# Performance work log

Measured on AMD Instinct MI355X. Metric: run time of the kernel, lower is better.

Reference implementation:

```python
import jax, jax.numpy as jnp
import numpy as np

V, D, H, H2 = 50000, 256, 128, 128
B, S, T1 = 8, 512, 101
GAMMA = 1.0

def setup_inputs():
    key = jax.random.key(0)
    ks = jax.random.split(key, 24)
    g = lambda i, shape: jax.random.normal(ks[i], shape, jnp.float32) * 0.05
    z = lambda n: jnp.zeros((n,), jnp.float32)
    return dict(
        text=jax.random.randint(ks[0], (B, S), 0, V),
        text_length=jax.random.randint(ks[1], (B,), S // 2, S + 1),
        summary=jax.random.randint(ks[2], (B, T1), 0, V),
        summary_length=jax.random.randint(ks[3], (B,), 20, T1 + 1),
        word_vectors=g(4, (V, D)),
        Wih_f=g(5, (4 * H, D)), Whh_f=g(6, (4 * H, H)), bih_f=z(4 * H), bhh_f=z(4 * H),
        Wih_b=g(7, (4 * H, D)), Whh_b=g(8, (4 * H, H)), bih_b=z(4 * H), bhh_b=z(4 * H),
        Wdih=g(9, (4 * H, D)), Wdhh=g(10, (4 * H, H)), bdih=z(4 * H), bdhh=z(4 * H),
        W1=g(11, (H2, 3 * H + 1)), b1=z(H2),
        W2=g(12, (1, H2)), b2=z(1),
        Wl=g(13, (V, 3 * H)), bl=z(V),
    )

def _lstm_cell(x, h, c, Wih, Whh, bih, bhh):
    # torch gate order: i, f, g, o
    gates = x @ Wih.T + h @ Whh.T + bih + bhh
    i, f, g, o = jnp.split(gates, 4, axis=-1)
    c_new = jax.nn.sigmoid(f) * c + jax.nn.sigmoid(i) * jnp.tanh(g)
    h_new = jax.nn.sigmoid(o) * jnp.tanh(c_new)
    return h_new, c_new

def _masked_lstm(x, mask, Wih, Whh, bih, bhh):
    # emulate packed sequence: state frozen and output zeroed past each length
    Bsz, Hh = x.shape[0], Whh.shape[1]
    def step(carry, inp):
        h, c = carry
        xt, mt = inp
        h_new, c_new = _lstm_cell(xt, h, c, Wih, Whh, bih, bhh)
        m = mt[:, None]
        return (jnp.where(m, h_new, h), jnp.where(m, c_new, c)), jnp.where(m, h_new, 0.0)
    init = (jnp.zeros((Bsz, Hh), x.dtype), jnp.zeros((Bsz, Hh), x.dtype))
    (h, c), out = jax.lax.scan(step, init, (x.transpose(1, 0, 2), mask.T))
    return out.transpose(1, 0, 2), h, c  # out: [B,S,H]

def _forward(text, text_length, summary, summary_length, word_vectors, Wih_f, Whh_f, bih_f, bhh_f, Wih_b, Whh_b, bih_b, bhh_b, Wdih, Wdhh, bdih, bdhh, W1, b1, W2, b2, Wl, bl):
    Bsz, Slen = text.shape
    pos = jnp.arange(Slen)
    mask = pos[None, :] < text_length[:, None]  # [B,S]
    emb = word_vectors[text]  # [B,S,D]
    # bidirectional encoder (layer 0 fwd state initializes decoder, as h[:,0])
    out_f, h0, c0 = _masked_lstm(emb, mask, Wih_f, Whh_f, bih_f, bhh_f)
    ridx = jnp.where(mask, text_length[:, None] - 1 - pos[None, :], pos[None, :])
    x_rev = jnp.take_along_axis(emb, ridx[:, :, None], axis=1)
    out_r, _, _ = _masked_lstm(x_rev, mask, Wih_b, Whh_b, bih_b, bhh_b)
    out_b = jnp.take_along_axis(out_r, ridx[:, :, None], axis=1) * mask[:, :, None]
    text_states = jnp.concatenate([out_f, out_b], -1)  # [B,S,2H]

    T = summary.shape[1] - 1
    def dec_step(carry, inp):
        h, c, cov, loss = carry
        tok_t, tok_tp1, valid = inp
        x = word_vectors[tok_t]
        h_new, c_new = _lstm_cell(x, h, c, Wdih, Wdhh, bdih, bdhh)
        hs = jnp.broadcast_to(h_new[:, None, :], (text_states.shape[0], text_states.shape[1], h_new.shape[-1]))
        feats = jnp.concatenate([text_states, hs, cov[:, :, None]], -1)  # [B,S,3H+1]
        hid = jnp.tanh(jnp.einsum('bsf,hf->bsh', feats, W1) + b1)
        scores = jnp.einsum('bsh,oh->bso', hid, W2)[..., 0] + b2[0]  # [B,S]
        attn = jax.nn.softmax(scores, axis=-1)
        context = jnp.einsum('bs,bsd->bd', attn, text_states)  # [B,2H]
        logits = jnp.concatenate([context, h_new], -1) @ Wl.T + bl
        logp = jax.nn.log_softmax(logits, -1)
        nll = -jnp.take_along_axis(logp, tok_tp1[:, None], axis=1)[:, 0]
        cov_loss = jnp.minimum(cov, attn).sum(-1)  # min over cat([cov, attn], -2), summed
        step_loss = jnp.where(valid, nll + GAMMA * cov_loss, 0.0).sum()
        vm = valid[:, None]
        h = jnp.where(vm, h_new, h)
        c = jnp.where(vm, c_new, c)
        cov = cov + jnp.where(vm, attn, 0.0)  # coverage accumulated every step in supervised path
        return (h, c, cov, loss + step_loss), None
    tok_t = summary[:, :-1].T  # [T,B]
    tok_tp1 = summary[:, 1:].T
    valid = summary_length[None, :] > (jnp.arange(T)[:, None] + 1)  # summary_length - t - 1 > 0
    carry0 = (h0, c0, jnp.zeros((text_states.shape[0], text_states.shape[1]), jnp.float32), jnp.zeros((), jnp.float32))
    (h, c, cov, loss), _ = jax.lax.scan(dec_step, carry0, (tok_t, tok_tp1, valid))
    return loss / T

def reference(text, text_length, summary, summary_length, word_vectors, Wih_f, Whh_f, bih_f, bhh_f, Wih_b, Whh_b, bih_b, bhh_b, Wdih, Wdhh, bdih, bdhh, W1, b1, W2, b2, Wl, bl):
    return _forward(text, text_length, summary, summary_length, word_vectors, Wih_f, Whh_f, bih_f, bhh_f, Wih_b, Whh_b, bih_b, bhh_b, Wdih, Wdhh, bdih, bdhh, W1, b1, W2, b2, Wl, bl)
```

## Files before the change

### kernel.cpp

```cpp
#include <hip/hip_runtime.h>
#include <hip/hip_bf16.h>

#define VV 50000
#define DD 256
#define HH 128
#define G4 512
#define BB 8
#define SS 512
#define TT 100
#define T1 101
#define GAMMA 1.0f
#define LOG2E 1.44269504f
#define CGB 224
#define TPB 14
#define NBLK (17+CGB)

#define KB 10
#define NAB (TT/KB)
#define NIT (NAB+3)
#define AT_M 31
#define CX_M 31
#define HN_M 31
#define CV_M 63
#define PM_M 31

__device__ inline float rcpf_(float x){
#if __has_builtin(__builtin_amdgcn_rcpf)
  return __builtin_amdgcn_rcpf(x);
#else
  return 1.0f/x;
#endif
}
__device__ inline float exp2f_(float x){
#if __has_builtin(__builtin_amdgcn_exp2f)
  return __builtin_amdgcn_exp2f(x);
#else
  return exp2f(x);
#endif
}
__device__ inline float log2f_(float x){
#if __has_builtin(__builtin_amdgcn_logf)
  return __builtin_amdgcn_logf(x);
#else
  return log2f(x);
#endif
}
__device__ inline float fexp(float x){ return exp2f_(x*LOG2E); }
__device__ inline float sigf(float x){ return rcpf_(1.f + exp2f_(-x*LOG2E)); }
__device__ inline float tanh_(float x){
  float e = exp2f_(x*(2.0f*LOG2E));
  return 1.0f - 2.0f*rcpf_(e+1.0f);
}
__device__ inline unsigned short f2bf(float x){
  unsigned u = __float_as_uint(x);
  return (unsigned short)((u + 0x7fffu + ((u>>16)&1u)) >> 16);
}
__device__ inline float bf2f(unsigned short s){ return __uint_as_float(((unsigned)s)<<16); }
__device__ inline float bfrnd(float x){
  return __uint_as_float((__float_as_uint(x)+0x8000u)&0xffff0000u);
}
__device__ inline unsigned pack2rq(float a, float b){
#if __has_builtin(__builtin_amdgcn_perm)
  unsigned ua = __float_as_uint(a) + 0x8000u;
  unsigned ub = __float_as_uint(b) + 0x8000u;
  return __builtin_amdgcn_perm(ub, ua, 0x07060302u);
#else
  unsigned ra = (__float_as_uint(a)+0x8000u)>>16;
  unsigned rb = (__float_as_uint(b)+0x8000u)>>16;
  return ra | (rb<<16);
#endif
}

typedef __attribute__((ext_vector_type(2))) _Float16 h2v;
typedef __attribute__((ext_vector_type(8))) short bfrag;
typedef __attribute__((ext_vector_type(4))) float cfrag;

__device__ inline unsigned packh2(float a, float b){
  unsigned short ha = __builtin_bit_cast(unsigned short, (_Float16)a);
  unsigned short hb = __builtin_bit_cast(unsigned short, (_Float16)b);
  return (unsigned)ha | ((unsigned)hb<<16);
}
__device__ inline float fdot2_(unsigned a, unsigned b, float c){
#if __has_builtin(__builtin_amdgcn_fdot2)
  return __builtin_amdgcn_fdot2(__builtin_bit_cast(h2v, a), __builtin_bit_cast(h2v, b), c, false);
#else
  h2v av = __builtin_bit_cast(h2v, a), bv = __builtin_bit_cast(h2v, b);
  return c + (float)av.x*(float)bv.x + (float)av.y*(float)bv.y;
#endif
}
__device__ inline float hlo(unsigned u){ return (float)__builtin_bit_cast(h2v, u).x; }
__device__ inline float hhi(unsigned u){ return (float)__builtin_bit_cast(h2v, u).y; }

__device__ inline void gbar(unsigned* bar){
  __syncthreads();
  if (threadIdx.x == 0){
    __threadfence();
    int g = blockIdx.x & 7;
    unsigned gsz = (unsigned)((NBLK + 7 - g) >> 3);
    unsigned gen = __hip_atomic_load(bar+576, __ATOMIC_RELAXED, __HIP_MEMORY_SCOPE_AGENT);
    unsigned old = __hip_atomic_fetch_add(bar+64*g, 1u, __ATOMIC_ACQ_REL, __HIP_MEMORY_SCOPE_AGENT);
    if (old == gsz-1u){
      __hip_atomic_store(bar+64*g, 0u, __ATOMIC_RELAXED, __HIP_MEMORY_SCOPE_AGENT);
      unsigned go = __hip_atomic_fetch_add(bar+512, 1u, __ATOMIC_ACQ_REL, __HIP_MEMORY_SCOPE_AGENT);
      if (go == 7u){
        __hip_atomic_store(bar+512, 0u, __ATOMIC_RELAXED, __HIP_MEMORY_SCOPE_AGENT);
        __hip_atomic_fetch_add(bar+576, 1u, __ATOMIC_RELEASE, __HIP_MEMORY_SCOPE_AGENT);
      } else {
        while (__hip_atomic_load(bar+576, __ATOMIC_RELAXED, __HIP_MEMORY_SCOPE_AGENT) == gen)
          __builtin_amdgcn_s_sleep(2);
      }
    } else {
      while (__hip_atomic_load(bar+576, __ATOMIC_RELAXED, __HIP_MEMORY_SCOPE_AGENT) == gen)
        __builtin_amdgcn_s_sleep(2);
    }
    __threadfence();
  }
  __syncthreads();
}

__global__ void __launch_bounds__(256) k_prep_small(
    const float* Wih_f, const float* Wih_b, const float* Whh_f, const float* Whh_b,
    const float* W1, const float* Wdhh,
    float* WihT_f, float* WihT_b, unsigned* W2T_f, unsigned* W2T_b,
    float* W1aT, float* W1c, unsigned* W1h2, unsigned* Wdh2T){
  int i = blockIdx.x*256 + threadIdx.x;
  if (i < 131072){ int k = i>>9, j = i&511; WihT_f[i] = Wih_f[j*DD + k]; return; }
  i -= 131072;
  if (i < 131072){ int k = i>>9, j = i&511; WihT_b[i] = Wih_b[j*DD + k]; return; }
  i -= 131072;
  if (i < 32768){ int k2 = i>>9, j = i&511;
    W2T_f[i] = packh2(Whh_f[j*HH + 2*k2], Whh_f[j*HH + 2*k2+1]); return; }
  i -= 32768;
  if (i < 32768){ int k2 = i>>9, j = i&511;
    W2T_b[i] = packh2(Whh_b[j*HH + 2*k2], Whh_b[j*HH + 2*k2+1]); return; }
  i -= 32768;
  if (i < 32768){ int d = i>>7, k = i&127; W1aT[i] = W1[k*385 + d]; return; }
  i -= 32768;
  if (i < 128){ W1c[i] = W1[i*385 + 384]; return; }
  i -= 128;
  if (i < 8192){ int j2 = i>>7, col = i&127;
    W1h2[i] = packh2(W1[col*385 + 256 + 2*j2], W1[col*385 + 256 + 2*j2+1]); return; }
  i -= 8192;
  if (i < 32768){ int q = i>>9, jj = i&511;
    Wdh2T[i] = packh2(Wdhh[jj*HH + 2*q], Wdhh[jj*HH + 2*q+1]); return; }
}

__global__ void __launch_bounds__(512) k_xd(const int* summary, const float* wv,
    const float* Wdih, const float* bdih, const float* bdhh,
    float* Xd, unsigned* bar){
  __shared__ float xsl[8][256];
  int t = blockIdx.x, tid = threadIdx.x;
  for (int f=tid; f<2048; f+=512){
    int b = f>>8, k = f&255;
    xsl[b][k] = wv[(size_t)summary[b*T1 + t]*DD + k];
  }
  if (blockIdx.x==0){ for (int f=tid; f<1024; f+=512) bar[f] = 0u; }
  __syncthreads();
  int jj = tid;
  float base = bdih[jj] + bdhh[jj];
  const float4* wr = (const float4*)(Wdih + (size_t)jj*DD);
  float acc[8];
  #pragma unroll
  for (int b=0;b<8;b++) acc[b]=0.f;
  for (int q=0;q<64;q++){
    float4 w = wr[q];
    #pragma unroll
    for (int b=0;b<8;b++)
      acc[b] += w.x*xsl[b][4*q] + w.y*xsl[b][4*q+1] + w.z*xsl[b][4*q+2] + w.w*xsl[b][4*q+3];
  }
  #pragma unroll
  for (int b=0;b<8;b++) Xd[((size_t)t*BB + b)*G4 + jj] = base + acc[b];
}

__global__ void k_embed(const int* text, const int* tlen, const float* wv,
                        float* emb, int* ridx){
  int blk = blockIdx.x;
  int b = blk>>9, s = blk&511;
  int tok = text[blk];
  const float4* src = (const float4*)(wv + (size_t)tok*DD);
  float4* dst = (float4*)(emb + (size_t)blk*DD);
  dst[threadIdx.x] = src[threadIdx.x];
  if (threadIdx.x==0){ int len = tlen[b]; ridx[blk] = (s < len) ? (len-1-s) : s; }
}

__global__ void __launch_bounds__(256) k_xgemm(const float* emb, const int* ridx,
    const float* WihT, const float* bi, const float* bh, float* X, int rev){
  __shared__ float e_l[8][256];
  int tid = threadIdx.x;
  int g0 = blockIdx.x*8;
  int b = g0>>9;
  for (int r=0;r<8;r++){
    int s = (g0+r)&511;
    int src = rev ? ridx[b*SS + s] : s;
    e_l[r][tid] = emb[((size_t)(b*SS+src))*DD + tid];
  }
  __syncthreads();
  int j0 = tid, j1 = tid+256;
  float acc0[8], acc1[8];
  #pragma unroll
  for (int r=0;r<8;r++){ acc0[r]=0.f; acc1[r]=0.f; }
  for (int k=0;k<256;k++){
    float w0 = WihT[k*G4 + j0];
    float w1 = WihT[k*G4 + j1];
    #pragma unroll
    for (int r=0;r<8;r++){ float e = e_l[r][k]; acc0[r] += e*w0; acc1[r] += e*w1; }
  }
  float bb0 = bi[j0]+bh[j0], bb1 = bi[j1]+bh[j1];
  for (int r=0;r<8;r++){
    X[((size_t)(g0+r))*G4 + j0] = acc0[r] + bb0;
    X[((size_t)(g0+r))*G4 + j1] = acc1[r] + bb1;
  }
}

__global__ void __launch_bounds__(512) k_encoder(const float* Xf, const float* Xb,
    const unsigned* W2Tf, const unsigned* W2Tb, const int* tlen,
    float* out_f, float* out_r, float* h0, float* c0){
  __shared__ float g_l[512];
  __shared__ __align__(16) unsigned h2_l[64];
  int tid = threadIdx.x;
  int b = blockIdx.x, dir = blockIdx.y;
  const float* X = dir ? Xb : Xf;
  const unsigned* WT = dir ? W2Tb : W2Tf;
  float* out = dir ? out_r : out_f;
  unsigned w[64];
  #pragma unroll
  for (int k2=0;k2<64;k2++) w[k2] = WT[k2*G4 + tid];
  if (tid < 64) h2_l[tid] = 0u;
  float creg = 0.f, hreg = 0.f;
  int len = tlen[b];
  __syncthreads();
  for (int t0=0;t0<len;t0+=8){
    float x8[8];
    #pragma unroll
    for (int i=0;i<8;i++) x8[i] = X[(size_t)(b*SS+t0+i)*G4 + tid];
    float out8[8];
    #pragma unroll
    for (int i=0;i<8;i++){
      int t = t0+i;
      if (t >= len) break;
      float a0 = x8[i], a1 = 0.f, a2 = 0.f, a3 = 0.f;
      const uint4* h4 = (const uint4*)h2_l;
      #pragma unroll
      for (int q=0;q<16;q++){
        uint4 hv = h4[q];
        a0 = fdot2_(w[4*q+0], hv.x, a0);
        a1 = fdot2_(w[4*q+1], hv.y, a1);
        a2 = fdot2_(w[4*q+2], hv.z, a2);
        a3 = fdot2_(w[4*q+3], hv.w, a3);
      }
      g_l[tid] = (a0+a1)+(a2+a3);
      __syncthreads();
      if (tid < 128){
        float ii = sigf(g_l[tid]);
        float ff = sigf(g_l[128+tid]);
        float gg = tanh_(g_l[256+tid]);
        float oo = sigf(g_l[384+tid]);
        creg = ff*creg + ii*gg;
        float hn = oo*tanh_(creg);
        out8[i] = hn;
        hreg = hn;
        ((_Float16*)h2_l)[tid] = (_Float16)hn;
      }
      __syncthreads();
    }
    if (tid < 128){
      int nend = (len - t0 < 8) ? (len - t0) : 8;
      #pragma unroll 8
      for (int i=0;i<nend;i++) out[((size_t)(b*SS+t0+i))*HH + tid] = out8[i];
    }
  }
  if (dir==0 && tid<128){ h0[b*HH+tid]=hreg; c0[b*HH+tid]=creg; }
  for (int f = tid; f < (SS-len)*HH; f += 512){
    int s = len + (f>>7), j = f&127;
    out[((size_t)(b*SS+s))*HH + j] = 0.f;
  }
}

__global__ void __launch_bounds__(256) k_post(const float* out_f, const float* out_r,
    const int* ridx, const float* W1aT, unsigned* ts_h, unsigned* TS1Th){
  __shared__ float ts_l[128*33 + 64];
  int tid = threadIdx.x;
  int b = blockIdx.x, chunk = blockIdx.y;
  int s0 = chunk*32;
  for (int it=0; it<32; ++it){
    int s = s0 + it;
    int d = tid;
    float v;
    if (d < 128) v = out_f[((size_t)(b*SS+s))*HH + d];
    else        v = out_r[((size_t)(b*SS + ridx[b*SS+s]))*HH + (d-128)];
    ts_l[it*256 + d] = v;
  }
  __syncthreads();
  for (int f=tid; f<16*256; f+=256){
    int it2 = f>>8, d = f&255;
    unsigned p = packh2(ts_l[(2*it2)*256 + d], ts_l[(2*it2+1)*256 + d]);
    ts_h[((((size_t)b*2 + (s0>>8))*128) + (((s0&255)>>1) + it2))*256 + d] = p;
  }
  int k = tid & 127, half = tid >> 7;
  float acc[16];
  #pragma unroll
  for (int i=0;i<16;i++) acc[i]=0.f;
  for (int d=0;d<256;d++){
    float w = W1aT[d*128 + k];
    #pragma unroll
    for (int i=0;i<16;i++) acc[i] += ts_l[(half*16+i)*256 + d]*w;
  }
  __syncthreads();
  #pragma unroll
  for (int i=0;i<16;i++) ts_l[k*33 + half*16 + i] = acc[i];
  __syncthreads();
  for (int f=tid; f<64*32; f+=256){
    int k2 = f>>5, sl = f&31;
    unsigned p = packh2(ts_l[(2*k2)*33 + sl], ts_l[(2*k2+1)*33 + sl]);
    TS1Th[((size_t)b*64 + k2)*512 + (s0 + sl)] = p;
  }
}

struct PArgs {
  const int* summary; const int* slen;
  const float* Xd; const unsigned* TS1Th; const unsigned* ts_h;
  const unsigned* W1h2g; const float* W1c; const float* W2; const float* b1;
  const unsigned* Wdh2T; const float* Wl; const float* bl;
  const float* h0; const float* c0;
  float* hn; float* ctx; float* attn; float* covloss;
  float* pm; float* ps; unsigned* bar; float* out;
};

struct __align__(16) LdsAB {
  unsigned W1h2[8192];
  float gates[512];
  float hnl[128], hml[128];
  unsigned hn2[64], hm2[64];
  float4 uhwc[64];
  float2 w2p[64];
  float wredB[8], wredC[8];
};
struct LdsCG { unsigned short xs[16*392]; float rm[64], rs[64]; };
struct LdsCTX { float at[512]; float part[512]; };
struct LdsCB { float tgt[32*BB]; float red[8]; float loss; };
union LdsU { LdsAB ab; LdsCG cg; LdsCTX cx; LdsCB cb; };

__global__ void __launch_bounds__(512,2) k_decode(PArgs a){
  __shared__ LdsU L;
  int bid = blockIdx.x, tid = threadIdx.x;

  if (bid < 8){
    int b = bid;
    int slenb = a.slen[b];
    float b1r = (tid < 128) ? a.b1[tid] : 0.f;
    if (tid < 64){
      L.ab.uhwc[tid] = make_float4(0.f, 0.f, a.W1c[2*tid], a.W1c[2*tid+1]);
      L.ab.w2p[tid]  = make_float2(a.W2[2*tid], a.W2[2*tid+1]);
    }
    for (int f=tid; f<8192; f+=512) L.ab.W1h2[f] = a.W1h2g[f];
    unsigned ts2[64];
    #pragma unroll
    for (int k2=0;k2<64;k2++) ts2[k2] = a.TS1Th[((size_t)b*64 + k2)*512 + tid];
    unsigned wdh[64];
    #pragma unroll
    for (int q=0;q<64;q++) wdh[q] = a.Wdh2T[q*512 + tid];
    float creg = 0.f, hmreg = 0.f;
    if (tid < 128){
      creg  = a.c0[b*HH+tid];
      hmreg = a.h0[b*HH+tid];
      L.ab.hml[tid] = hmreg;
    }
    float cv = 0.f;
    __syncthreads();
    if (tid < 64) L.ab.hm2[tid] = packh2(L.ab.hml[2*tid], L.ab.hml[2*tid+1]);
    __syncthreads();
    {
      const uint4* h4 = (const uint4*)L.ab.hm2;
      float g0 = a.Xd[(size_t)0*BB*G4 + b*G4 + tid], g1 = 0.f, g2 = 0.f, g3 = 0.f;
      #pragma unroll
      for (int q=0;q<16;q++){
        uint4 hv = h4[q];
        g0 = fdot2_(wdh[4*q+0], hv.x, g0);
        g1 = fdot2_(wdh[4*q+1], hv.y, g1);
        g2 = fdot2_(wdh[4*q+2], hv.z, g2);
        g3 = fdot2_(wdh[4*q+3], hv.w, g3);
      }
      L.ab.gates[tid] = (g0+g1)+(g2+g3);
    }
    __syncthreads();

    for (int it=0; it<NIT; ++it){
      if (it < NAB){
        #pragma unroll 1
        for (int j=0;j<KB;j++){
          int t = KB*it + j;
          if (j) __syncthreads();
          if (t >= TT) break;
          int tn = (t+1 < TT) ? t+1 : 0;
          float xdn = a.Xd[(size_t)tn*BB*G4 + b*G4 + tid];
          bool valid = (slenb > t+1);
          if (tid < 128){
            float gi = L.ab.gates[tid];
            float gf = L.ab.gates[128+tid];
            float gg = L.ab.gates[256+tid];
            float go = L.ab.gates[384+tid];
            float ii = sigf(gi), ff = sigf(gf), g2 = tanh_(gg), oo = sigf(go);
            float cn = ff*creg + ii*g2;
            float hv = oo*tanh_(cn);
            if (valid) creg = cn;
            hmreg = valid ? hv : hmreg;
            L.ab.hnl[tid] = hv;
            L.ab.hml[tid] = hmreg;
            a.hn[((size_t)(t&HN_M)*BB + b)*HH + tid] = hv;
          }
          __syncthreads();
          if (tid < 64){
            L.ab.hn2[tid] = packh2(L.ab.hnl[2*tid], L.ab.hnl[2*tid+1]);
            L.ab.hm2[tid] = packh2(L.ab.hml[2*tid], L.ab.hml[2*tid+1]);
          }
          __syncthreads();
          if (tid < 128){
            const uint4* n4 = (const uint4*)L.ab.hn2;
            float u0 = b1r, u1 = 0.f, u2 = 0.f, u3 = 0.f;
            #pragma unroll
            for (int q=0;q<16;q++){
              uint4 nv = n4[q];
              u0 = fdot2_(L.ab.W1h2[(4*q+0)*128+tid], nv.x, u0);
              u1 = fdot2_(L.ab.W1h2[(4*q+1)*128+tid], nv.y, u1);
              u2 = fdot2_(L.ab.W1h2[(4*q+2)*128+tid], nv.z, u2);
              u3 = fdot2_(L.ab.W1h2[(4*q+3)*128+tid], nv.w, u3);
            }
            ((float*)L.ab.uhwc)[(tid>>1)*4 + (tid&1)] = (u0+u1)+(u2+u3);
          }
          __syncthreads();
          float sc0 = 0.f, sc1 = 0.f;
          #pragma unroll
          for (int k2=0;k2<64;k2++){
            unsigned tp = ts2[k2];
            float4 uw  = L.ab.uhwc[k2];
            float2 w2v = L.ab.w2p[k2];
            float p0 = hlo(tp) + uw.x + cv*uw.z;
            float p1 = hhi(tp) + uw.y + cv*uw.w;
            sc0 += tanh_(p0)*w2v.x;
            sc1 += tanh_(p1)*w2v.y;
          }
          float e = fexp(sc0 + sc1);
          int wid = tid>>6;
          float es = e;
          #pragma unroll
          for (int off=32;off>=1;off>>=1) es += __shfl_xor(es, off, 64);
          if ((tid&63)==0) L.ab.wredB[wid] = es;
          __syncthreads();
          float ssum = 0.f;
          #pragma unroll
          for (int w8=0;w8<8;w8++) ssum += L.ab.wredB[w8];
          float at = e * rcpf_(ssum);
          a.attn[((size_t)(t&AT_M)*BB + b)*SS + tid] = at;
          float cl = fminf(cv, at);
          #pragma unroll
          for (int off=32;off>=1;off>>=1) cl += __shfl_xor(cl, off, 64);
          if ((tid&63)==0) L.ab.wredC[wid] = cl;
          __syncthreads();
          if (tid==0){
            float cvs = 0.f;
            #pragma unroll
            for (int w8=0;w8<8;w8++) cvs += L.ab.wredC[w8];
            a.covloss[(t&CV_M)*BB + b] = cvs;
          }
          if (valid) cv += at;
          if (t+1 < TT){
            const uint4* h4 = (const uint4*)L.ab.hm2;
            float g0 = xdn, g1 = 0.f, g2 = 0.f, g3 = 0.f;
            #pragma unroll
            for (int q=0;q<16;q++){
              uint4 hv = h4[q];
              g0 = fdot2_(wdh[4*q+0], hv.x, g0);
              g1 = fdot2_(wdh[4*q+1], hv.y, g1);
              g2 = fdot2_(wdh[4*q+2], hv.z, g2);
              g3 = fdot2_(wdh[4*q+3], hv.w, g3);
            }
            __syncthreads();
            L.ab.gates[tid] = (g0+g1)+(g2+g3);
          }
        }
      }
      gbar(a.bar);
    }
  } else if (bid < 16){
    int b = bid-8;
    int d = tid & 255, half = tid >> 8;
    unsigned tsr[128];
    #pragma unroll
    for (int s2=0;s2<128;s2++)
      tsr[s2] = a.ts_h[((((size_t)b*2 + half)*128) + s2)*256 + d];
    for (int it=0; it<NIT; ++it){
      if (it >= 1 && it <= NAB){
        #pragma unroll 1
        for (int j=0;j<KB;j++){
          int s = KB*(it-1) + j;
          if (s >= TT) break;
          L.cx.at[tid] = a.attn[((size_t)(s&AT_M)*BB + b)*SS + tid];
          __syncthreads();
          float acc = 0.f;
          const float* ap = L.cx.at + half*256;
          #pragma unroll
          for (int s2=0;s2<128;s2++){
            float2 av = *(const float2*)&ap[2*s2];
            unsigned tp = tsr[s2];
            acc += hlo(tp)*av.x + hhi(tp)*av.y;
          }
          L.cx.part[tid] = acc;
          __syncthreads();
          if (tid < 256)
            a.ctx[((size_t)(s&CX_M)*BB + b)*256 + tid] = L.cx.part[tid] + L.cx.part[256+tid];
        }
      }
      gbar(a.bar);
    }
  } else if (bid == 16){
    int b = tid >> 6, l = tid & 63;
    int slenb = a.slen[b];
    if (tid == 0) L.cb.loss = 0.f;
    __syncthreads();
    for (int it=0; it<NIT; ++it){
      #pragma unroll 1
      for (int j=0;j<KB;j++){
        int ts = KB*(it-2) + j;
        if (ts >= 0 && ts < TT){
          int tp = a.summary[b*T1 + ts+1];
          float acc = 0.f;
          #pragma unroll
          for (int i=0;i<6;i++){
            int k = l + 64*i;
            float x = (k < 256) ? a.ctx[((size_t)(ts&CX_M)*BB + b)*256 + k]
                                : a.hn[((size_t)(ts&HN_M)*BB + b)*HH + (k-256)];
            float w = a.Wl[(size_t)tp*384 + k];
            acc += bf2f(f2bf(x)) * bfrnd(w);
          }
          #pragma unroll
          for (int off=32;off>=1;off>>=1) acc += __shfl_xor(acc, off, 64);
          if (l==0) L.cb.tgt[(ts&31)*BB + b] = acc + a.bl[tp];
        }
        int cs = KB*(it-3) + j;
        if (cs >= 0 && cs < TT){
          int slot = cs&PM_M;
          const float* pmp = a.pm + (size_t)slot*BB*CGB + b*CGB;
          const float* psp = a.ps + (size_t)slot*BB*CGB + b*CGB;
          float m = -1e30f;
          for (int jb=l; jb<CGB; jb+=64) m = fmaxf(m, pmp[jb]);
          #pragma unroll
          for (int off=32;off>=1;off>>=1) m = fmaxf(m, __shfl_xor(m, off, 64));
          float s = 0.f;
          for (int jb=l; jb<CGB; jb+=64) s += psp[jb]*fexp(pmp[jb]-m);
          #pragma unroll
          for (int off=32;off>=1;off>>=1) s += __shfl_xor(s, off, 64);
          __syncthreads();
          if (l==0){
            float lse = m + log2f_(s)*0.6931472f;
            bool val = slenb > cs+1;
            L.cb.red[b] = val ? (lse - L.cb.tgt[(cs&31)*BB+b] + GAMMA*a.covloss[(cs&CV_M)*BB+b]) : 0.f;
          }
          __syncthreads();
          if (tid==0){
            float sum = 0.f;
            #pragma unroll
            for (int b2=0;b2<BB;b2++) sum += L.cb.red[b2];
            L.cb.loss += sum;
          }
        }
      }
      if (it==NIT-1 && tid==0) a.out[0] = L.cb.loss*(1.0f/TT);
      gbar(a.bar);
    }
  } else {
    int cb = bid-17;
    int lane = tid & 63, wid = tid >> 6;
    int quad = lane >> 4, col = lane & 15;
    uint4 wreg[24];
    float biasv[2];
    bool nOK[2];
    #pragma unroll
    for (int lt=0; lt<2; lt++){
      int lti = lt*8 + wid;
      bool gv = (lti < TPB);
      int g = cb*TPB + (gv ? lti : 0);
      int n = g*16 + col;
      int nc = (n < VV) ? n : (VV-1);
      const float* wr0 = a.Wl + (size_t)nc*384 + quad*8;
      #pragma unroll
      for (int ks=0; ks<12; ks++){
        float4 w0 = *((const float4*)(wr0 + ks*32));
        float4 w1 = *((const float4*)(wr0 + ks*32 + 4));
        wreg[lt*12+ks] = make_uint4(pack2rq(w0.x,w0.y), pack2rq(w0.z,w0.w),
                                    pack2rq(w1.x,w1.y), pack2rq(w1.z,w1.w));
      }
      nOK[lt] = gv && (n < VV);
      biasv[lt] = nOK[lt] ? a.bl[n] : 0.f;
    }
    for (int it=0; it<NIT; ++it){
      if (it >= 2 && it <= NAB+1){
        #pragma unroll 1
        for (int j=0;j<KB;j++){
          int s = KB*(it-2) + j;
          if (s >= TT) break;
          for (int f=tid; f<16*384; f+=512){
            int m2 = f/384, k = f - m2*384;
            float v = 0.f;
            if (m2 < 8) v = (k < 256) ? a.ctx[((size_t)(s&CX_M)*BB + m2)*256 + k]
                                      : a.hn[((size_t)(s&HN_M)*BB + m2)*HH + (k-256)];
            L.cg.xs[m2*392 + k] = f2bf(v);
          }
          __syncthreads();
          const unsigned short* ap = L.cg.xs + col*392 + quad*8;
          float mr[4], sr[4];
          #pragma unroll
          for (int r=0;r<4;r++){ mr[r] = -1e30f; sr[r] = 0.f; }
          #pragma unroll
          for (int lt=0; lt<2; lt++){
            cfrag acc; acc.x=0.f; acc.y=0.f; acc.z=0.f; acc.w=0.f;
            #pragma unroll
            for (int ks=0; ks<12; ks++){
              bfrag af = *((const bfrag*)(ap + ks*32));
              bfrag bf = __builtin_bit_cast(bfrag, wreg[lt*12+ks]);
              acc = __builtin_amdgcn_mfma_f32_16x16x32_bf16(af, bf, acc, 0,0,0);
            }
            #pragma unroll
            for (int r=0;r<4;r++){
              int mrow = quad*4 + r;
              float v = (mrow < 8 && nOK[lt]) ? (acc[r]+biasv[lt]) : -1e30f;
              float nm = fmaxf(mr[r], v);
              float ev = (v <= -1e29f) ? 0.f : fexp(v-nm);
              sr[r] = sr[r]*fexp(mr[r]-nm) + ev;
              mr[r] = nm;
            }
          }
          #pragma unroll
          for (int off=1; off<16; off<<=1){
            #pragma unroll
            for (int r=0;r<4;r++){
              float m2 = __shfl_xor(mr[r], off, 64);
              float s2 = __shfl_xor(sr[r], off, 64);
              float nm = fmaxf(mr[r], m2);
              sr[r] = sr[r]*fexp(mr[r]-nm) + s2*fexp(m2-nm);
              mr[r] = nm;
            }
          }
          if (col==0 && quad<2){
            #pragma unroll
            for (int r=0;r<4;r++){
              L.cg.rm[wid*8 + quad*4 + r] = mr[r];
              L.cg.rs[wid*8 + quad*4 + r] = sr[r];
            }
          }
          __syncthreads();
          if (tid < 8){
            float M = -1e30f, S = 0.f;
            #pragma unroll
            for (int w8=0; w8<8; w8++){
              float m2 = L.cg.rm[w8*8+tid], s2 = L.cg.rs[w8*8+tid];
              float nm = fmaxf(M, m2);
              S = S*fexp(M-nm) + s2*fexp(m2-nm);
              M = nm;
            }
            a.pm[(size_t)(s&PM_M)*BB*CGB + tid*CGB + cb] = M;
            a.ps[(size_t)(s&PM_M)*BB*CGB + tid*CGB + cb] = S;
          }
        }
      }
      gbar(a.bar);
    }
  }
}

extern "C" void kernel_launch(void* const* d_in, const int* in_sizes, int n_in,
                              void* d_out, int out_size, void* d_ws, size_t ws_size,
                              hipStream_t stream){
  const int* text      = (const int*)d_in[0];
  const int* tlen      = (const int*)d_in[1];
  const int* summary   = (const int*)d_in[2];
  const int* slen      = (const int*)d_in[3];
  const float* wv      = (const float*)d_in[4];
  const float* Wih_f   = (const float*)d_in[5];
  const float* Whh_f   = (const float*)d_in[6];
  const float* bih_f   = (const float*)d_in[7];
  const float* bhh_f   = (const float*)d_in[8];
  const float* Wih_b   = (const float*)d_in[9];
  const float* Whh_b   = (const float*)d_in[10];
  const float* bih_b   = (const float*)d_in[11];
  const float* bhh_b   = (const float*)d_in[12];
  const float* Wdih    = (const float*)d_in[13];
  const float* Wdhh    = (const float*)d_in[14];
  const float* bdih    = (const float*)d_in[15];
  const float* bdhh    = (const float*)d_in[16];
  const float* W1      = (const float*)d_in[17];
  const float* b1      = (const float*)d_in[18];
  const float* W2      = (const float*)d_in[19];
  const float* Wl      = (const float*)d_in[21];
  const float* bl      = (const float*)d_in[22];

  char* ws = (char*)d_ws;
  size_t off = 0;
  auto alloc = [&](size_t n)->void*{
    off = (off + 255) & ~(size_t)255;
    void* p = ws + off; off += n; return p;
  };

  unsigned* W1h2   = (unsigned*)alloc((size_t)8192*4);
  unsigned* Wdh2T  = (unsigned*)alloc((size_t)64*512*4);
  float*    Xd     = (float*)alloc((size_t)TT*BB*G4*4);
  unsigned* ts_h   = (unsigned*)alloc((size_t)BB*2*128*256*4);
  unsigned* TS1Th  = (unsigned*)alloc((size_t)BB*64*512*4);
  float* W1c       = (float*)alloc((size_t)128*4);
  float* h0        = (float*)alloc(BB*HH*4);
  float* c0        = (float*)alloc(BB*HH*4);
  float* hn        = (float*)alloc((size_t)(HN_M+1)*BB*HH*4);
  float* ctx       = (float*)alloc((size_t)(CX_M+1)*BB*256*4);
  float* attn      = (float*)alloc((size_t)(AT_M+1)*BB*SS*4);
  float* covloss   = (float*)alloc((size_t)(CV_M+1)*BB*4);
  float* pm        = (float*)alloc((size_t)(PM_M+1)*BB*CGB*4);
  float* ps        = (float*)alloc((size_t)(PM_M+1)*BB*CGB*4);
  unsigned* bar    = (unsigned*)alloc(4096);

  float* emb     = (float*)alloc((size_t)BB*SS*DD*4);
  float* Xf      = (float*)alloc(((size_t)BB*SS*G4 + 8*G4)*4);
  float* Xb      = (float*)alloc(((size_t)BB*SS*G4 + 8*G4)*4);
  float* WihT_f  = (float*)alloc((size_t)256*512*4);
  float* WihT_b  = (float*)alloc((size_t)256*512*4);
  unsigned* W2T_f= (unsigned*)alloc((size_t)64*512*4);
  unsigned* W2T_b= (unsigned*)alloc((size_t)64*512*4);
  float* out_f   = (float*)alloc((size_t)BB*SS*HH*4);
  float* out_r   = (float*)alloc((size_t)BB*SS*HH*4);
  float* W1aT    = (float*)alloc((size_t)256*128*4);
  int*   ridx    = (int*)  alloc((size_t)BB*SS*4);

  k_prep_small<<<1569,256,0,stream>>>(Wih_f,Wih_b,Whh_f,Whh_b,W1,Wdhh,
                                      WihT_f,WihT_b,W2T_f,W2T_b,W1aT,W1c,W1h2,Wdh2T);
  k_xd<<<TT,512,0,stream>>>(summary, wv, Wdih, bdih, bdhh, Xd, bar);
  k_embed<<<BB*SS,64,0,stream>>>(text, tlen, wv, emb, ridx);
  k_xgemm<<<512,256,0,stream>>>(emb, ridx, WihT_f, bih_f, bhh_f, Xf, 0);
  k_xgemm<<<512,256,0,stream>>>(emb, ridx, WihT_b, bih_b, bhh_b, Xb, 1);
  k_encoder<<<dim3(8,2),512,0,stream>>>(Xf,Xb,W2T_f,W2T_b,tlen,out_f,out_r,h0,c0);
  k_post<<<dim3(8,16),256,0,stream>>>(out_f,out_r,ridx,W1aT,ts_h,TS1Th);

  PArgs a;
  a.summary=summary; a.slen=slen;
  a.Xd=Xd; a.TS1Th=TS1Th; a.ts_h=ts_h;
  a.W1h2g=W1h2; a.W1c=W1c; a.W2=W2; a.b1=b1;
  a.Wdh2T=Wdh2T; a.Wl=Wl; a.bl=bl;
  a.h0=h0; a.c0=c0;
  a.hn=hn; a.ctx=ctx; a.attn=attn; a.covloss=covloss;
  a.pm=pm; a.ps=ps; a.bar=bar; a.out=(float*)d_out;

  k_decode<<<NBLK,512,0,stream>>>(a);
}
```

Baseline: 1.492 ms.

## Split decoder attention score across paired blocks with flag-based handoff

Adds 8 helper blocks, one per batch row, that compute the attention scores for hidden units 72..127 while the main recurrent block computes units 0..71. The two blocks exchange partial scores and the packed hidden state through global memory, synchronised by per-batch release/acquire tags. The serial per-step attention tanh loop on the critical path gets shorter. The macro-step size KB also grows from 10 to 25 and the ring buffers are enlarged to match, so grid barriers happen less often. In exchange, every step now pays two cross-block polling handoffs.

```diff
diff --git a/kernel.cpp b/kernel.cpp
--- a/kernel.cpp
+++ b/kernel.cpp
@@ -13,16 +13,22 @@
 #define LOG2E 1.44269504f
 #define CGB 224
 #define TPB 14
-#define NBLK (17+CGB)
-
-#define KB 10
+#define NBLK (17+8+CGB)
+
+#define KB 25
 #define NAB (TT/KB)
 #define NIT (NAB+3)
-#define AT_M 31
-#define CX_M 31
-#define HN_M 31
-#define CV_M 63
-#define PM_M 31
+#define AT_M 63
+#define CX_M 63
+#define HN_M 127
+#define CV_M 127
+#define PM_M 63
+
+#define A_K2 36
+#define B_K2 (64-A_K2)
+#define THN 640
+#define TGA 768
+#define TGB 896
 
 __device__ inline float rcpf_(float x){
 #if __has_builtin(__builtin_amdgcn_rcpf)
@@ -90,6 +96,16 @@
 }
 __device__ inline float hlo(unsigned u){ return (float)__builtin_bit_cast(h2v, u).x; }
 __device__ inline float hhi(unsigned u){ return (float)__builtin_bit_cast(h2v, u).y; }
+
+__device__ inline void tag_pub(unsigned* tag, unsigned v){
+  __threadfence();
+  __hip_atomic_store(tag, v, __ATOMIC_RELEASE, __HIP_MEMORY_SCOPE_AGENT);
+}
+__device__ inline void tag_poll(unsigned* tag, unsigned v){
+  while (__hip_atomic_load(tag, __ATOMIC_RELAXED, __HIP_MEMORY_SCOPE_AGENT) < v)
+    __builtin_amdgcn_s_sleep(1);
+  __threadfence();
+}
 
 __device__ inline void gbar(unsigned* bar){
   __syncthreads();
@@ -324,6 +340,7 @@
   const float* h0; const float* c0;
   float* hn; float* ctx; float* attn; float* covloss;
   float* pm; float* ps; unsigned* bar; float* out;
+  unsigned* hnG; float* scA; float* scB;
 };
 
 struct __align__(16) LdsAB {
@@ -337,7 +354,7 @@
 };
 struct LdsCG { unsigned short xs[16*392]; float rm[64], rs[64]; };
 struct LdsCTX { float at[512]; float part[512]; };
-struct LdsCB { float tgt[32*BB]; float red[8]; float loss; };
+struct LdsCB { float tgt[64*BB]; float red[8]; float loss; };
 union LdsU { LdsAB ab; LdsCG cg; LdsCTX cx; LdsCB cb; };
 
 __global__ void __launch_bounds__(512,2) k_decode(PArgs a){
@@ -347,15 +364,15 @@
   if (bid < 8){
     int b = bid;
     int slenb = a.slen[b];
-    float b1r = (tid < 128) ? a.b1[tid] : 0.f;
+    float b1r = (tid < 2*A_K2) ? a.b1[tid] : 0.f;
     if (tid < 64){
       L.ab.uhwc[tid] = make_float4(0.f, 0.f, a.W1c[2*tid], a.W1c[2*tid+1]);
       L.ab.w2p[tid]  = make_float2(a.W2[2*tid], a.W2[2*tid+1]);
     }
     for (int f=tid; f<8192; f+=512) L.ab.W1h2[f] = a.W1h2g[f];
-    unsigned ts2[64];
-    #pragma unroll
-    for (int k2=0;k2<64;k2++) ts2[k2] = a.TS1Th[((size_t)b*64 + k2)*512 + tid];
+    unsigned ts2[A_K2];
+    #pragma unroll
+    for (int k2=0;k2<A_K2;k2++) ts2[k2] = a.TS1Th[((size_t)b*64 + k2)*512 + tid];
     unsigned wdh[64];
     #pragma unroll
     for (int q=0;q<64;q++) wdh[q] = a.Wdh2T[q*512 + tid];
@@ -410,11 +427,14 @@
           }
           __syncthreads();
           if (tid < 64){
-            L.ab.hn2[tid] = packh2(L.ab.hnl[2*tid], L.ab.hnl[2*tid+1]);
+            unsigned pn = packh2(L.ab.hnl[2*tid], L.ab.hnl[2*tid+1]);
+            L.ab.hn2[tid] = pn;
+            a.hnG[((size_t)b*2 + (t&1))*64 + tid] = pn;
             L.ab.hm2[tid] = packh2(L.ab.hml[2*tid], L.ab.hml[2*tid+1]);
           }
           __syncthreads();
-          if (tid < 128){
+          if (tid == 504) tag_pub(a.bar + THN + 16*b, (unsigned)(t+1));
+          if (tid < 2*A_K2){
             const uint4* n4 = (const uint4*)L.ab.hn2;
             float u0 = b1r, u1 = 0.f, u2 = 0.f, u3 = 0.f;
             #pragma unroll
@@ -430,7 +450,7 @@
           __syncthreads();
           float sc0 = 0.f, sc1 = 0.f;
           #pragma unroll
-          for (int k2=0;k2<64;k2++){
+          for (int k2=0;k2<A_K2;k2++){
             unsigned tp = ts2[k2];
             float4 uw  = L.ab.uhwc[k2];
             float2 w2v = L.ab.w2p[k2];
@@ -439,7 +459,14 @@
             sc0 += tanh_(p0)*w2v.x;
             sc1 += tanh_(p1)*w2v.y;
           }
-          float e = fexp(sc0 + sc1);
+          float scA = sc0 + sc1;
+          a.scA[((size_t)b*2 + (t&1))*512 + tid] = scA;
+          __syncthreads();
+          if (tid == 504) tag_pub(a.bar + TGA + 16*b, (unsigned)(t+1));
+          if (tid == 0)   tag_poll(a.bar + TGB + 16*b, (unsigned)(t+1));
+          __syncthreads();
+          float sc = scA + a.scB[((size_t)b*2 + (t&1))*512 + tid];
+          float e = fexp(sc);
           int wid = tid>>6;
           float es = e;
           #pragma unroll
@@ -534,7 +561,7 @@
           }
           #pragma unroll
           for (int off=32;off>=1;off>>=1) acc += __shfl_xor(acc, off, 64);
-          if (l==0) L.cb.tgt[(ts&31)*BB + b] = acc + a.bl[tp];
+          if (l==0) L.cb.tgt[(ts&63)*BB + b] = acc + a.bl[tp];
         }
         int cs = KB*(it-3) + j;
         if (cs >= 0 && cs < TT){
@@ -553,7 +580,7 @@
           if (l==0){
             float lse = m + log2f_(s)*0.6931472f;
             bool val = slenb > cs+1;
-            L.cb.red[b] = val ? (lse - L.cb.tgt[(cs&31)*BB+b] + GAMMA*a.covloss[(cs&CV_M)*BB+b]) : 0.f;
+            L.cb.red[b] = val ? (lse - L.cb.tgt[(cs&63)*BB+b] + GAMMA*a.covloss[(cs&CV_M)*BB+b]) : 0.f;
           }
           __syncthreads();
           if (tid==0){
@@ -567,8 +594,84 @@
       if (it==NIT-1 && tid==0) a.out[0] = L.cb.loss*(1.0f/TT);
       gbar(a.bar);
     }
+  } else if (bid < 25){
+    int b = bid-17;
+    int slenb = a.slen[b];
+    float b1r2 = (tid < 2*B_K2) ? a.b1[2*A_K2 + tid] : 0.f;
+    if (tid < 64){
+      L.ab.uhwc[tid] = make_float4(0.f, 0.f, a.W1c[2*tid], a.W1c[2*tid+1]);
+      L.ab.w2p[tid]  = make_float2(a.W2[2*tid], a.W2[2*tid+1]);
+    }
+    for (int f=tid; f<8192; f+=512) L.ab.W1h2[f] = a.W1h2g[f];
+    unsigned ts2b[B_K2];
+    #pragma unroll
+    for (int i=0;i<B_K2;i++) ts2b[i] = a.TS1Th[((size_t)b*64 + (A_K2+i))*512 + tid];
+    float cv = 0.f;
+    __syncthreads();
+    for (int it=0; it<NIT; ++it){
+      if (it < NAB){
+        #pragma unroll 1
+        for (int j=0;j<KB;j++){
+          int t = KB*it + j;
+          if (t >= TT) break;
+          if (tid == 0) tag_poll(a.bar + THN + 16*b, (unsigned)(t+1));
+          __syncthreads();
+          if (tid < 64) L.ab.hn2[tid] = a.hnG[((size_t)b*2 + (t&1))*64 + tid];
+          __syncthreads();
+          if (tid < 2*B_K2){
+            int col = 2*A_K2 + tid;
+            const uint4* n4 = (const uint4*)L.ab.hn2;
+            float u0 = b1r2, u1 = 0.f, u2 = 0.f, u3 = 0.f;
+            #pragma unroll
+            for (int q=0;q<16;q++){
+              uint4 nv = n4[q];
+              u0 = fdot2_(L.ab.W1h2[(4*q+0)*128+col], nv.x, u0);
+              u1 = fdot2_(L.ab.W1h2[(4*q+1)*128+col], nv.y, u1);
+              u2 = fdot2_(L.ab.W1h2[(4*q+2)*128+col], nv.z, u2);
+              u3 = fdot2_(L.ab.W1h2[(4*q+3)*128+col], nv.w, u3);
+            }
+            ((float*)L.ab.uhwc)[(col>>1)*4 + (col&1)] = (u0+u1)+(u2+u3);
+          }
+          __syncthreads();
+          float sc0 = 0.f, sc1 = 0.f;
+          #pragma unroll
+          for (int i=0;i<B_K2;i++){
+            int k2 = A_K2 + i;
+            unsigned tp = ts2b[i];
+            float4 uw  = L.ab.uhwc[k2];
+            float2 w2v = L.ab.w2p[k2];
+            float p0 = hlo(tp) + uw.x + cv*uw.z;
+            float p1 = hhi(tp) + uw.y + cv*uw.w;
+            sc0 += tanh_(p0)*w2v.x;
+            sc1 += tanh_(p1)*w2v.y;
+          }
+          float scB = sc0 + sc1;
+          a.scB[((size_t)b*2 + (t&1))*512 + tid] = scB;
+          __syncthreads();
+          if (tid == 504) tag_pub(a.bar + TGB + 16*b, (unsigned)(t+1));
+          if (tid == 0)   tag_poll(a.bar + TGA + 16*b, (unsigned)(t+1));
+          __syncthreads();
+          float sc = a.scA[((size_t)b*2 + (t&1))*512 + tid] + scB;
+          float e = fexp(sc);
+          int wid = tid>>6;
+          float es = e;
+          #pragma unroll
+          for (int off=32;off>=1;off>>=1) es += __shfl_xor(es, off, 64);
+          if ((tid&63)==0) L.ab.wredB[wid] = es;
+          __syncthreads();
+          float ssum = 0.f;
+          #pragma unroll
+          for (int w8=0;w8<8;w8++) ssum += L.ab.wredB[w8];
+          float at = e * rcpf_(ssum);
+          bool valid = (slenb > t+1);
+          if (valid) cv += at;
+          __syncthreads();
+        }
+      }
+      gbar(a.bar);
+    }
   } else {
-    int cb = bid-17;
+    int cb = bid-25;
     int lane = tid & 63, wid = tid >> 6;
     int quad = lane >> 4, col = lane & 15;
     uint4 wreg[24];
@@ -715,6 +818,9 @@
   float* pm        = (float*)alloc((size_t)(PM_M+1)*BB*CGB*4);
   float* ps        = (float*)alloc((size_t)(PM_M+1)*BB*CGB*4);
   unsigned* bar    = (unsigned*)alloc(4096);
+  unsigned* hnG    = (unsigned*)alloc((size_t)BB*2*64*4);
+  float* scA       = (float*)alloc((size_t)BB*2*512*4);
+  float* scB       = (float*)alloc((size_t)BB*2*512*4);
 
   float* emb     = (float*)alloc((size_t)BB*SS*DD*4);
   float* Xf      = (float*)alloc(((size_t)BB*SS*G4 + 8*G4)*4);
@@ -745,6 +851,7 @@
   a.h0=h0; a.c0=c0;
   a.hn=hn; a.ctx=ctx; a.attn=attn; a.covloss=covloss;
   a.pm=pm; a.ps=ps; a.bar=bar; a.out=(float*)d_out;
+  a.hnG=hnG; a.scA=scA; a.scB=scB;
 
   k_decode<<<NBLK,512,0,stream>>>(a);
 }
```

Measured after the change: 1.697 ms. 1.14x slower.

## Split per-batch attention across two blocks with pairwise softmax-sum exchange

Applied to the files above, without the earlier changes.

Each decoder batch row is now handled by two blocks instead of one. Each thread computes half of the 64-step attention score reduction for one sequence position, and the halves are combined with a lane shuffle. The two blocks exchange partial softmax denominators through 64-bit tagged atomic slots, and coverage loss is stored per half. The next-step gate matvec is now interleaved into the score loop rather than run after a barrier. This costs an inter-block spin handshake every step, extra redundant LSTM and W1 work in both blocks, and launch bounds lowered to 1 block per SM.

```diff
diff --git a/kernel.cpp b/kernel.cpp
--- a/kernel.cpp
+++ b/kernel.cpp
@@ -13,7 +13,7 @@
 #define LOG2E 1.44269504f
 #define CGB 224
 #define TPB 14
-#define NBLK (17+CGB)
+#define NBLK (25+CGB)
 
 #define KB 10
 #define NAB (TT/KB)
@@ -90,6 +90,16 @@
 }
 __device__ inline float hlo(unsigned u){ return (float)__builtin_bit_cast(h2v, u).x; }
 __device__ inline float hhi(unsigned u){ return (float)__builtin_bit_cast(h2v, u).y; }
+
+__device__ inline void pub64(unsigned long long* p, unsigned long long v){
+  __hip_atomic_store(p, v, __ATOMIC_RELEASE, __HIP_MEMORY_SCOPE_AGENT);
+}
+__device__ inline unsigned poll64(unsigned long long* p, unsigned hi){
+  unsigned long long v;
+  do { v = __hip_atomic_load(p, __ATOMIC_ACQUIRE, __HIP_MEMORY_SCOPE_AGENT); }
+  while ((unsigned)(v>>32) != hi);
+  return (unsigned)v;
+}
 
 __device__ inline void gbar(unsigned* bar){
   __syncthreads();
@@ -334,28 +344,32 @@
   float4 uhwc[64];
   float2 w2p[64];
   float wredB[8], wredC[8];
+  float ssumv;
 };
 struct LdsCG { unsigned short xs[16*392]; float rm[64], rs[64]; };
 struct LdsCTX { float at[512]; float part[512]; };
 struct LdsCB { float tgt[32*BB]; float red[8]; float loss; };
 union LdsU { LdsAB ab; LdsCG cg; LdsCTX cx; LdsCB cb; };
 
-__global__ void __launch_bounds__(512,2) k_decode(PArgs a){
+__global__ void __launch_bounds__(512,1) k_decode(PArgs a){
   __shared__ LdsU L;
   int bid = blockIdx.x, tid = threadIdx.x;
 
-  if (bid < 8){
-    int b = bid;
+  if (bid < 16){
+    int b = bid >> 1, half = bid & 1;
     int slenb = a.slen[b];
+    int kh = tid & 1;
+    int sg = half*256 + (tid >> 1);
+    unsigned long long* slots = (unsigned long long*)(a.bar + 640);
     float b1r = (tid < 128) ? a.b1[tid] : 0.f;
     if (tid < 64){
       L.ab.uhwc[tid] = make_float4(0.f, 0.f, a.W1c[2*tid], a.W1c[2*tid+1]);
       L.ab.w2p[tid]  = make_float2(a.W2[2*tid], a.W2[2*tid+1]);
     }
     for (int f=tid; f<8192; f+=512) L.ab.W1h2[f] = a.W1h2g[f];
-    unsigned ts2[64];
-    #pragma unroll
-    for (int k2=0;k2<64;k2++) ts2[k2] = a.TS1Th[((size_t)b*64 + k2)*512 + tid];
+    unsigned ts2[32];
+    #pragma unroll
+    for (int i=0;i<32;i++) ts2[i] = a.TS1Th[((size_t)b*64 + kh*32 + i)*512 + sg];
     unsigned wdh[64];
     #pragma unroll
     for (int q=0;q<64;q++) wdh[q] = a.Wdh2T[q*512 + tid];
@@ -406,7 +420,7 @@
             hmreg = valid ? hv : hmreg;
             L.ab.hnl[tid] = hv;
             L.ab.hml[tid] = hmreg;
-            a.hn[((size_t)(t&HN_M)*BB + b)*HH + tid] = hv;
+            if (half==0) a.hn[((size_t)(t&HN_M)*BB + b)*HH + tid] = hv;
           }
           __syncthreads();
           if (tid < 64){
@@ -429,9 +443,21 @@
           }
           __syncthreads();
           float sc0 = 0.f, sc1 = 0.f;
-          #pragma unroll
-          for (int k2=0;k2<64;k2++){
-            unsigned tp = ts2[k2];
+          float g0 = xdn, g1 = 0.f, g2 = 0.f, g3 = 0.f;
+          const uint4* h4 = (const uint4*)L.ab.hm2;
+          uint4 hv;
+          #pragma unroll
+          for (int i=0;i<32;i++){
+            if ((i&1)==0){
+              hv = h4[i>>1];
+              g0 = fdot2_(wdh[2*i],   hv.x, g0);
+              g1 = fdot2_(wdh[2*i+1], hv.y, g1);
+            } else {
+              g2 = fdot2_(wdh[2*i],   hv.z, g2);
+              g3 = fdot2_(wdh[2*i+1], hv.w, g3);
+            }
+            int k2 = kh*32 + i;
+            unsigned tp = ts2[i];
             float4 uw  = L.ab.uhwc[k2];
             float2 w2v = L.ab.w2p[k2];
             float p0 = hlo(tp) + uw.x + cv*uw.z;
@@ -439,19 +465,29 @@
             sc0 += tanh_(p0)*w2v.x;
             sc1 += tanh_(p1)*w2v.y;
           }
-          float e = fexp(sc0 + sc1);
+          L.ab.gates[tid] = (g0+g1)+(g2+g3);
+          float sc = sc0 + sc1;
+          sc += __shfl_xor(sc, 1, 64);
+          float e = fexp(sc);
+          float es = kh ? 0.f : e;
+          #pragma unroll
+          for (int off=32;off>=1;off>>=1) es += __shfl_xor(es, off, 64);
           int wid = tid>>6;
-          float es = e;
-          #pragma unroll
-          for (int off=32;off>=1;off>>=1) es += __shfl_xor(es, off, 64);
           if ((tid&63)==0) L.ab.wredB[wid] = es;
           __syncthreads();
-          float ssum = 0.f;
-          #pragma unroll
-          for (int w8=0;w8<8;w8++) ssum += L.ab.wredB[w8];
-          float at = e * rcpf_(ssum);
-          a.attn[((size_t)(t&AT_M)*BB + b)*SS + tid] = at;
-          float cl = fminf(cv, at);
+          if (tid==0){
+            float esH = 0.f;
+            #pragma unroll
+            for (int w8=0;w8<8;w8++) esH += L.ab.wredB[w8];
+            pub64(&slots[b*2+half],
+                  ((unsigned long long)(t+1)<<32) | (unsigned long long)__float_as_uint(esH));
+            unsigned ob = poll64(&slots[b*2+(half^1)], (unsigned)(t+1));
+            L.ab.ssumv = esH + __uint_as_float(ob);
+          }
+          __syncthreads();
+          float at = e * rcpf_(L.ab.ssumv);
+          if (kh==0) a.attn[((size_t)(t&AT_M)*BB + b)*SS + sg] = at;
+          float cl = kh ? 0.f : fminf(cv, at);
           #pragma unroll
           for (int off=32;off>=1;off>>=1) cl += __shfl_xor(cl, off, 64);
           if ((tid&63)==0) L.ab.wredC[wid] = cl;
@@ -460,29 +496,15 @@
             float cvs = 0.f;
             #pragma unroll
             for (int w8=0;w8<8;w8++) cvs += L.ab.wredC[w8];
-            a.covloss[(t&CV_M)*BB + b] = cvs;
+            a.covloss[((t&CV_M)*BB + b)*2 + half] = cvs;
           }
           if (valid) cv += at;
-          if (t+1 < TT){
-            const uint4* h4 = (const uint4*)L.ab.hm2;
-            float g0 = xdn, g1 = 0.f, g2 = 0.f, g3 = 0.f;
-            #pragma unroll
-            for (int q=0;q<16;q++){
-              uint4 hv = h4[q];
-              g0 = fdot2_(wdh[4*q+0], hv.x, g0);
-              g1 = fdot2_(wdh[4*q+1], hv.y, g1);
-              g2 = fdot2_(wdh[4*q+2], hv.z, g2);
-              g3 = fdot2_(wdh[4*q+3], hv.w, g3);
-            }
-            __syncthreads();
-            L.ab.gates[tid] = (g0+g1)+(g2+g3);
-          }
         }
       }
       gbar(a.bar);
     }
-  } else if (bid < 16){
-    int b = bid-8;
+  } else if (bid < 24){
+    int b = bid-16;
     int d = tid & 255, half = tid >> 8;
     unsigned tsr[128];
     #pragma unroll
@@ -512,7 +534,7 @@
       }
       gbar(a.bar);
     }
-  } else if (bid == 16){
+  } else if (bid == 24){
     int b = tid >> 6, l = tid & 63;
     int slenb = a.slen[b];
     if (tid == 0) L.cb.loss = 0.f;
@@ -553,7 +575,9 @@
           if (l==0){
             float lse = m + log2f_(s)*0.6931472f;
             bool val = slenb > cs+1;
-            L.cb.red[b] = val ? (lse - L.cb.tgt[(cs&31)*BB+b] + GAMMA*a.covloss[(cs&CV_M)*BB+b]) : 0.f;
+            float cvs = a.covloss[((cs&CV_M)*BB + b)*2 + 0]
+                      + a.covloss[((cs&CV_M)*BB + b)*2 + 1];
+            L.cb.red[b] = val ? (lse - L.cb.tgt[(cs&31)*BB+b] + GAMMA*cvs) : 0.f;
           }
           __syncthreads();
           if (tid==0){
@@ -568,7 +592,7 @@
       gbar(a.bar);
     }
   } else {
-    int cb = bid-17;
+    int cb = bid-25;
     int lane = tid & 63, wid = tid >> 6;
     int quad = lane >> 4, col = lane & 15;
     uint4 wreg[24];
@@ -711,7 +735,7 @@
   float* hn        = (float*)alloc((size_t)(HN_M+1)*BB*HH*4);
   float* ctx       = (float*)alloc((size_t)(CX_M+1)*BB*256*4);
   float* attn      = (float*)alloc((size_t)(AT_M+1)*BB*SS*4);
-  float* covloss   = (float*)alloc((size_t)(CV_M+1)*BB*4);
+  float* covloss   = (float*)alloc((size_t)(CV_M+1)*BB*2*4);
   float* pm        = (float*)alloc((size_t)(PM_M+1)*BB*CGB*4);
   float* ps        = (float*)alloc((size_t)(PM_M+1)*BB*CGB*4);
   unsigned* bar    = (unsigned*)alloc(4096);
```

Result: faster. 1.349 ms (-9.6%).
